# Optimization experiments

Hardware: AMD Instinct MI355X
Metric: run time of the kernel (lower is better)

Reference implementation:

```python
import jax, jax.numpy as jnp
import numpy as np

T, B, I, H = 512, 256, 256, 256


def setup_inputs() -> dict:
    key = jax.random.key(0)
    ks = jax.random.split(key, 4)
    s = 1.0 / np.sqrt(I + H)  # fan-in scaling like nn.Linear default
    return {
        "x": jax.random.normal(ks[0], (T, B, I), dtype=jnp.float32),
        "h": jnp.zeros((B, H), dtype=jnp.float32),
        "Wz_w": jax.random.normal(ks[1], (H, I + H), dtype=jnp.float32) * s,
        "Wz_b": jnp.zeros((H,), dtype=jnp.float32),
        "Wr_w": jax.random.normal(ks[2], (H, I + H), dtype=jnp.float32) * s,
        "Wr_b": jnp.zeros((H,), dtype=jnp.float32),
        "W_w": jax.random.normal(ks[3], (H, I + H), dtype=jnp.float32) * s,
        "W_b": jnp.zeros((H,), dtype=jnp.float32),
    }


def reference(x, h, Wz_w, Wz_b, Wr_w, Wr_b, W_w, W_b):
    # x: [T, B, I], h: [B, H]. Gate input order is cat(h, x) as in the torch code.
    def step(h, xt):
        gate = jnp.concatenate([h, xt], axis=1)              # [B, H+I]
        zt = jax.nn.sigmoid(gate @ Wz_w.T + Wz_b)            # [B, H]
        rt = jax.nn.sigmoid(gate @ Wr_w.T + Wr_b)            # [B, H]
        cand_in = jnp.concatenate([rt * h, xt], axis=1)      # [B, H+I]
        ht = (1.0 - zt) * h + zt * jnp.tanh(cand_in @ W_w.T + W_b)
        return ht, ht

    h_final, hAll = jax.lax.scan(step, h, x)                 # hAll: [T, B, H]
    return hAll, h_final
```

## Files before the change

### kernel.cpp

```cpp
#include <hip/hip_runtime.h>


typedef float f32x4 __attribute__((ext_vector_type(4)));
typedef short bf16x8 __attribute__((ext_vector_type(8)));

__device__ __forceinline__ unsigned short f2bf(float f) {
  union { float f; unsigned int u; } v; v.f = f;
  unsigned int u = v.u + 0x7fffu + ((v.u >> 16) & 1u);
  return (unsigned short)(u >> 16);
}
__device__ __forceinline__ float u2f(unsigned int u) {
  union { unsigned int u; float f; } v; v.u = u; return v.f;
}
__device__ __forceinline__ unsigned int cvt_pk_bf16(float lo, float hi) {
  unsigned int r;
  asm("v_cvt_pk_bf16_f32 %0, %1, %2" : "=v"(r) : "v"(lo), "v"(hi));
  return r;
}
__device__ __forceinline__ float sigmoid_f(float x) {
  return __builtin_amdgcn_rcpf(1.f + __expf(-x));
}
__device__ __forceinline__ float tanh_f(float x) {
  float e = __expf(2.f * x);
  return 1.f - 2.f * __builtin_amdgcn_rcpf(e + 1.f);
}
__device__ __forceinline__ f32x4 unpk(uint2 gv) {
  f32x4 a;
  a[0] = u2f(gv.x << 16); a[1] = u2f(gv.x & 0xffff0000u);
  a[2] = u2f(gv.y << 16); a[3] = u2f(gv.y & 0xffff0000u);
  return a;
}
__device__ __forceinline__ int frag_off(int j, int b) {
  return ((j >> 5) * 64 + ((j >> 3) & 3) * 16 + b) * 8 + (j & 7);
}

__global__ __launch_bounds__(256) void gru_gx_kernel(
    const float* __restrict__ x,
    const float* __restrict__ Wz, const float* __restrict__ Wr, const float* __restrict__ Wc,
    const float* __restrict__ bz, const float* __restrict__ br, const float* __restrict__ bc,
    unsigned short* __restrict__ gx)
{
  __shared__ __align__(16) unsigned short As[64][72];
  __shared__ __align__(16) unsigned short Bs[64][72];

  const int tid  = threadIdx.x;
  const int lane = tid & 63;
  const int wid  = tid >> 6;
  const int l15  = lane & 15;
  const int lg   = lane >> 4;
  const int m0   = blockIdx.x * 64;
  const int by   = blockIdx.y;
  const int gate = by >> 2;
  const int jb   = (by & 3) * 64;
  const float* W    = (gate == 0) ? Wz : ((gate == 1) ? Wr : Wc);
  const float* bias = (gate == 0) ? bz : ((gate == 1) ? br : bc);

  f32x4 acc[4];
  #pragma unroll
  for (int n = 0; n < 4; ++n) acc[n] = (f32x4){0.f, 0.f, 0.f, 0.f};

  for (int k0 = 0; k0 < 256; k0 += 64) {
    #pragma unroll
    for (int i = 0; i < 4; ++i) {
      int idx = tid + i * 256;
      int row = idx >> 4;
      int kq  = (idx & 15) << 2;
      float4 va = *(const float4*)(x + (size_t)(m0 + row) * 256 + k0 + kq);
      ushort4 ua; ua.x = f2bf(va.x); ua.y = f2bf(va.y); ua.z = f2bf(va.z); ua.w = f2bf(va.w);
      *(ushort4*)&As[row][kq] = ua;
      float4 vb = *(const float4*)(W + (size_t)(jb + row) * 512 + 256 + k0 + kq);
      ushort4 ub; ub.x = f2bf(vb.x); ub.y = f2bf(vb.y); ub.z = f2bf(vb.z); ub.w = f2bf(vb.w);
      *(ushort4*)&Bs[row][kq] = ub;
    }
    __syncthreads();
    #pragma unroll
    for (int ks = 0; ks < 64; ks += 32) {
      bf16x8 af = *(const bf16x8*)&As[wid * 16 + l15][ks + lg * 8];
      #pragma unroll
      for (int n = 0; n < 4; ++n) {
        bf16x8 bf = *(const bf16x8*)&Bs[n * 16 + l15][ks + lg * 8];
        acc[n] = __builtin_amdgcn_mfma_f32_16x16x32_bf16(af, bf, acc[n], 0, 0, 0);
      }
    }
    __syncthreads();
  }

  #pragma unroll
  for (int n = 0; n < 4; ++n) {
    float bv = bias[jb + n * 16 + l15];
    #pragma unroll
    for (int r = 0; r < 4; ++r) {
      As[wid * 16 + lg * 4 + r][n * 16 + l15] = f2bf(acc[n][r] + bv);
    }
  }
  __syncthreads();

  const int tt    = m0 >> 8;
  const int b0    = m0 & 255;
  const int jbase = by * 64;
  #pragma unroll
  for (int i = 0; i < 2; ++i) {
    int u    = tid + i * 256;
    int bg_l = u >> 7;
    int rem  = u & 127;
    int cb_l = rem >> 3;
    int bp   = rem & 7;
    int row0 = bg_l * 16 + bp * 2;
    uint2 lo = *(const uint2*)&As[row0][cb_l * 4];
    uint2 hi = *(const uint2*)&As[row0 + 1][cb_l * 4];
    uint4 val; val.x = lo.x; val.y = lo.y; val.z = hi.x; val.w = hi.y;
    size_t off = (((size_t)tt * 16 + (b0 >> 4) + bg_l) * 192 + (jbase >> 2) + cb_l) * 64
                 + (size_t)bp * 8;
    *(uint4*)(gx + off) = val;
  }
}

__global__ __launch_bounds__(512, 1) void gru_rec_kernel(
    const unsigned short* __restrict__ gx,
    const float* __restrict__ h0,
    const float* __restrict__ Wz, const float* __restrict__ Wr, const float* __restrict__ Wc,
    float* __restrict__ out)
{
  __shared__ __align__(16) float h_s[16][268];
  __shared__ __align__(16) float zt_s[16][268];
  __shared__ __align__(16) unsigned short hA[4096];
  __shared__ __align__(16) unsigned short rhA[4096];

  const int tid   = threadIdx.x;
  const int lane  = tid & 63;
  const int wid   = tid >> 6;
  const int l15   = lane & 15;
  const int lg    = lane >> 4;
  const int wg    = blockIdx.x;
  const int brow0 = wg * 16;

  bf16x8 w1[4][8];
  {
    const float* W  = (wid < 4) ? Wz : Wr;
    const int    cb = (wid & 3) * 64;
    #pragma unroll
    for (int n = 0; n < 4; ++n) {
      const int j = cb + n * 16 + l15;
      #pragma unroll
      for (int kk = 0; kk < 8; ++kk) {
        const int k = kk * 32 + lg * 8;
        const float* p = W + (size_t)j * 512 + k;
        float4 a = *(const float4*)p;
        float4 b = *(const float4*)(p + 4);
        bf16x8 f;
        f[0] = (short)f2bf(a.x); f[1] = (short)f2bf(a.y);
        f[2] = (short)f2bf(a.z); f[3] = (short)f2bf(a.w);
        f[4] = (short)f2bf(b.x); f[5] = (short)f2bf(b.y);
        f[6] = (short)f2bf(b.z); f[7] = (short)f2bf(b.w);
        w1[n][kk] = f;
      }
    }
  }
  bf16x8 w2[2][8];
  {
    const int cb = wid * 32;
    #pragma unroll
    for (int n = 0; n < 2; ++n) {
      const int j = cb + n * 16 + l15;
      #pragma unroll
      for (int kk = 0; kk < 8; ++kk) {
        const int k = kk * 32 + lg * 8;
        const float* p = Wc + (size_t)j * 512 + k;
        float4 a = *(const float4*)p;
        float4 b = *(const float4*)(p + 4);
        bf16x8 f;
        f[0] = (short)f2bf(a.x); f[1] = (short)f2bf(a.y);
        f[2] = (short)f2bf(a.z); f[3] = (short)f2bf(a.w);
        f[4] = (short)f2bf(b.x); f[5] = (short)f2bf(b.y);
        f[6] = (short)f2bf(b.z); f[7] = (short)f2bf(b.w);
        w2[n][kk] = f;
      }
    }
  }

  for (int idx = tid; idx < 16 * 256; idx += 512) {
    int r = idx >> 8, c = idx & 255;
    float v = h0[(size_t)(brow0 + r) * 256 + c];
    h_s[r][c] = v;
    hA[frag_off(c, r)] = f2bf(v);
  }

  uint2 g1[4], g2[2];
  {
    const size_t tb = (size_t)wg * 12288;
    #pragma unroll
    for (int n = 0; n < 4; ++n)
      g1[n] = *(const uint2*)(gx + tb + (size_t)(wid * 16 + n * 4 + lg) * 64 + l15 * 4);
    #pragma unroll
    for (int n = 0; n < 2; ++n)
      g2[n] = *(const uint2*)(gx + tb + (size_t)(128 + wid * 8 + n * 4 + lg) * 64 + l15 * 4);
  }
  __syncthreads();

  for (int t = 0; t < 512; ++t) {
    const int tn = (t < 511) ? (t + 1) : 511;
    const size_t tbn = ((size_t)tn * 16 + wg) * 12288;

    const int cb1 = wid * 64;
    f32x4 acc[4];
    #pragma unroll
    for (int n = 0; n < 4; ++n) acc[n] = unpk(g1[n]);
    #pragma unroll
    for (int n = 0; n < 4; ++n)
      g1[n] = *(const uint2*)(gx + tbn + (size_t)(wid * 16 + n * 4 + lg) * 64 + l15 * 4);

    #pragma unroll
    for (int kk = 0; kk < 8; ++kk) {
      bf16x8 hf = *(const bf16x8*)&hA[kk * 512 + lane * 8];
      #pragma unroll
      for (int n = 0; n < 4; ++n)
        acc[n] = __builtin_amdgcn_mfma_f32_16x16x32_bf16(w1[n][kk], hf, acc[n], 0, 0, 0);
    }
    if (wid < 4) {
      #pragma unroll
      for (int n = 0; n < 4; ++n) {
        const int c0 = cb1 + n * 16 + lg * 4;
        f32x4 zv;
        #pragma unroll
        for (int r = 0; r < 4; ++r) zv[r] = sigmoid_f(acc[n][r]);
        *(f32x4*)&zt_s[l15][c0] = zv;
      }
    } else {
      #pragma unroll
      for (int n = 0; n < 4; ++n) {
        const int c0h = (cb1 - 256) + n * 16 + lg * 4;
        f32x4 hv = *(const f32x4*)&h_s[l15][c0h];
        float rh0 = sigmoid_f(acc[n][0]) * hv[0];
        float rh1 = sigmoid_f(acc[n][1]) * hv[1];
        float rh2 = sigmoid_f(acc[n][2]) * hv[2];
        float rh3 = sigmoid_f(acc[n][3]) * hv[3];
        uint2 pk; pk.x = cvt_pk_bf16(rh0, rh1); pk.y = cvt_pk_bf16(rh2, rh3);
        *(uint2*)&rhA[frag_off(c0h, l15)] = pk;
      }
    }
    asm volatile("s_waitcnt lgkmcnt(0)" ::: "memory");
    __builtin_amdgcn_s_barrier();
    __builtin_amdgcn_sched_barrier(0);

    f32x4 acc2[2];
    #pragma unroll
    for (int n = 0; n < 2; ++n) acc2[n] = unpk(g2[n]);
    #pragma unroll
    for (int n = 0; n < 2; ++n)
      g2[n] = *(const uint2*)(gx + tbn + (size_t)(128 + wid * 8 + n * 4 + lg) * 64 + l15 * 4);

    #pragma unroll
    for (int kk = 0; kk < 8; ++kk) {
      bf16x8 rf = *(const bf16x8*)&rhA[kk * 512 + lane * 8];
      #pragma unroll
      for (int n = 0; n < 2; ++n)
        acc2[n] = __builtin_amdgcn_mfma_f32_16x16x32_bf16(w2[n][kk], rf, acc2[n], 0, 0, 0);
    }
    #pragma unroll
    for (int n = 0; n < 2; ++n) {
      const int j0 = wid * 32 + n * 16 + lg * 4;
      f32x4 zv = *(const f32x4*)&zt_s[l15][j0];
      f32x4 hp = *(const f32x4*)&h_s[l15][j0];
      f32x4 ht;
      #pragma unroll
      for (int r = 0; r < 4; ++r) {
        float th = tanh_f(acc2[n][r]);
        ht[r] = hp[r] + zv[r] * (th - hp[r]);
      }
      *(f32x4*)(out + (size_t)t * 65536 + (size_t)(brow0 + l15) * 256 + j0) = ht;
      if (t == 511)
        *(f32x4*)(out + (size_t)33554432 + (size_t)(brow0 + l15) * 256 + j0) = ht;
      *(f32x4*)&h_s[l15][j0] = ht;
      uint2 pk; pk.x = cvt_pk_bf16(ht[0], ht[1]); pk.y = cvt_pk_bf16(ht[2], ht[3]);
      *(uint2*)&hA[frag_off(j0, l15)] = pk;
    }
    asm volatile("s_waitcnt lgkmcnt(0)" ::: "memory");
    __builtin_amdgcn_s_barrier();
    __builtin_amdgcn_sched_barrier(0);
  }
}

extern "C" void kernel_launch(void* const* d_in, const int* in_sizes, int n_in,
                              void* d_out, int out_size, void* d_ws, size_t ws_size,
                              hipStream_t stream) {
  const float* x  = (const float*)d_in[0];
  const float* h0 = (const float*)d_in[1];
  const float* Wz = (const float*)d_in[2];
  const float* bz = (const float*)d_in[3];
  const float* Wr = (const float*)d_in[4];
  const float* br = (const float*)d_in[5];
  const float* Wc = (const float*)d_in[6];
  const float* bc = (const float*)d_in[7];
  float* out = (float*)d_out;
  unsigned short* gxbuf = (unsigned short*)d_ws;

  dim3 gridA(2048, 12);
  gru_gx_kernel<<<gridA, 256, 0, stream>>>(x, Wz, Wr, Wc, bz, br, bc, gxbuf);
  gru_rec_kernel<<<16, 512, 0, stream>>>(gxbuf, h0, Wz, Wr, Wc, out);
}
```

Baseline: 1.246 ms.

## Split recurrent GRU work across 16 waves per block instead of 8

Doubles the recurrent kernel's block size from 512 to 1024 threads. Each wave now handles half as many gate columns: two 16-column tiles for z/r and one for the candidate. This shortens the serial per-step MFMA chain and elementwise work per wave, aiming to cut latency on the 512-step critical path. In exchange, the two block-wide barriers per step cover twice as many waves, and only 16 blocks are launched, so most of the GPU stays idle.

```diff
diff --git a/kernel.cpp b/kernel.cpp
--- a/kernel.cpp
+++ b/kernel.cpp
@@ -115,7 +115,7 @@
   }
 }
 
-__global__ __launch_bounds__(512, 1) void gru_rec_kernel(
+__global__ __launch_bounds__(1024, 1) void gru_rec_kernel(
     const unsigned short* __restrict__ gx,
     const float* __restrict__ h0,
     const float* __restrict__ Wz, const float* __restrict__ Wr, const float* __restrict__ Wc,
@@ -129,17 +129,19 @@
   const int tid   = threadIdx.x;
   const int lane  = tid & 63;
   const int wid   = tid >> 6;
+  const int w7    = wid & 7;
+  const int zr    = wid >> 3;
   const int l15   = lane & 15;
   const int lg    = lane >> 4;
   const int wg    = blockIdx.x;
   const int brow0 = wg * 16;
 
-  bf16x8 w1[4][8];
+  bf16x8 w1[2][8];
   {
-    const float* W  = (wid < 4) ? Wz : Wr;
-    const int    cb = (wid & 3) * 64;
-    #pragma unroll
-    for (int n = 0; n < 4; ++n) {
+    const float* W  = zr ? Wr : Wz;
+    const int    cb = w7 * 32;
+    #pragma unroll
+    for (int n = 0; n < 2; ++n) {
       const int j = cb + n * 16 + l15;
       #pragma unroll
       for (int kk = 0; kk < 8; ++kk) {
@@ -156,44 +158,38 @@
       }
     }
   }
-  bf16x8 w2[2][8];
+  bf16x8 w2[8];
   {
-    const int cb = wid * 32;
-    #pragma unroll
-    for (int n = 0; n < 2; ++n) {
-      const int j = cb + n * 16 + l15;
-      #pragma unroll
-      for (int kk = 0; kk < 8; ++kk) {
-        const int k = kk * 32 + lg * 8;
-        const float* p = Wc + (size_t)j * 512 + k;
-        float4 a = *(const float4*)p;
-        float4 b = *(const float4*)(p + 4);
-        bf16x8 f;
-        f[0] = (short)f2bf(a.x); f[1] = (short)f2bf(a.y);
-        f[2] = (short)f2bf(a.z); f[3] = (short)f2bf(a.w);
-        f[4] = (short)f2bf(b.x); f[5] = (short)f2bf(b.y);
-        f[6] = (short)f2bf(b.z); f[7] = (short)f2bf(b.w);
-        w2[n][kk] = f;
-      }
-    }
-  }
-
-  for (int idx = tid; idx < 16 * 256; idx += 512) {
+    const int j = wid * 16 + l15;
+    #pragma unroll
+    for (int kk = 0; kk < 8; ++kk) {
+      const int k = kk * 32 + lg * 8;
+      const float* p = Wc + (size_t)j * 512 + k;
+      float4 a = *(const float4*)p;
+      float4 b = *(const float4*)(p + 4);
+      bf16x8 f;
+      f[0] = (short)f2bf(a.x); f[1] = (short)f2bf(a.y);
+      f[2] = (short)f2bf(a.z); f[3] = (short)f2bf(a.w);
+      f[4] = (short)f2bf(b.x); f[5] = (short)f2bf(b.y);
+      f[6] = (short)f2bf(b.z); f[7] = (short)f2bf(b.w);
+      w2[kk] = f;
+    }
+  }
+
+  for (int idx = tid; idx < 16 * 256; idx += 1024) {
     int r = idx >> 8, c = idx & 255;
     float v = h0[(size_t)(brow0 + r) * 256 + c];
     h_s[r][c] = v;
     hA[frag_off(c, r)] = f2bf(v);
   }
 
-  uint2 g1[4], g2[2];
+  uint2 g1[2], g2;
   {
     const size_t tb = (size_t)wg * 12288;
     #pragma unroll
-    for (int n = 0; n < 4; ++n)
-      g1[n] = *(const uint2*)(gx + tb + (size_t)(wid * 16 + n * 4 + lg) * 64 + l15 * 4);
-    #pragma unroll
     for (int n = 0; n < 2; ++n)
-      g2[n] = *(const uint2*)(gx + tb + (size_t)(128 + wid * 8 + n * 4 + lg) * 64 + l15 * 4);
+      g1[n] = *(const uint2*)(gx + tb + (size_t)(zr * 64 + w7 * 8 + n * 4 + lg) * 64 + l15 * 4);
+    g2 = *(const uint2*)(gx + tb + (size_t)(128 + wid * 4 + lg) * 64 + l15 * 4);
   }
   __syncthreads();
 
@@ -201,25 +197,24 @@
     const int tn = (t < 511) ? (t + 1) : 511;
     const size_t tbn = ((size_t)tn * 16 + wg) * 12288;
 
-    const int cb1 = wid * 64;
-    f32x4 acc[4];
-    #pragma unroll
-    for (int n = 0; n < 4; ++n) acc[n] = unpk(g1[n]);
-    #pragma unroll
-    for (int n = 0; n < 4; ++n)
-      g1[n] = *(const uint2*)(gx + tbn + (size_t)(wid * 16 + n * 4 + lg) * 64 + l15 * 4);
+    f32x4 acc[2];
+    #pragma unroll
+    for (int n = 0; n < 2; ++n) acc[n] = unpk(g1[n]);
+    #pragma unroll
+    for (int n = 0; n < 2; ++n)
+      g1[n] = *(const uint2*)(gx + tbn + (size_t)(zr * 64 + w7 * 8 + n * 4 + lg) * 64 + l15 * 4);
 
     #pragma unroll
     for (int kk = 0; kk < 8; ++kk) {
       bf16x8 hf = *(const bf16x8*)&hA[kk * 512 + lane * 8];
       #pragma unroll
-      for (int n = 0; n < 4; ++n)
+      for (int n = 0; n < 2; ++n)
         acc[n] = __builtin_amdgcn_mfma_f32_16x16x32_bf16(w1[n][kk], hf, acc[n], 0, 0, 0);
     }
-    if (wid < 4) {
-      #pragma unroll
-      for (int n = 0; n < 4; ++n) {
-        const int c0 = cb1 + n * 16 + lg * 4;
+    if (zr == 0) {
+      #pragma unroll
+      for (int n = 0; n < 2; ++n) {
+        const int c0 = w7 * 32 + n * 16 + lg * 4;
         f32x4 zv;
         #pragma unroll
         for (int r = 0; r < 4; ++r) zv[r] = sigmoid_f(acc[n][r]);
@@ -227,8 +222,8 @@
       }
     } else {
       #pragma unroll
-      for (int n = 0; n < 4; ++n) {
-        const int c0h = (cb1 - 256) + n * 16 + lg * 4;
+      for (int n = 0; n < 2; ++n) {
+        const int c0h = w7 * 32 + n * 16 + lg * 4;
         f32x4 hv = *(const f32x4*)&h_s[l15][c0h];
         float rh0 = sigmoid_f(acc[n][0]) * hv[0];
         float rh1 = sigmoid_f(acc[n][1]) * hv[1];
@@ -242,29 +237,22 @@
     __builtin_amdgcn_s_barrier();
     __builtin_amdgcn_sched_barrier(0);
 
-    f32x4 acc2[2];
-    #pragma unroll
-    for (int n = 0; n < 2; ++n) acc2[n] = unpk(g2[n]);
-    #pragma unroll
-    for (int n = 0; n < 2; ++n)
-      g2[n] = *(const uint2*)(gx + tbn + (size_t)(128 + wid * 8 + n * 4 + lg) * 64 + l15 * 4);
+    f32x4 acc2 = unpk(g2);
+    g2 = *(const uint2*)(gx + tbn + (size_t)(128 + wid * 4 + lg) * 64 + l15 * 4);
 
     #pragma unroll
     for (int kk = 0; kk < 8; ++kk) {
       bf16x8 rf = *(const bf16x8*)&rhA[kk * 512 + lane * 8];
-      #pragma unroll
-      for (int n = 0; n < 2; ++n)
-        acc2[n] = __builtin_amdgcn_mfma_f32_16x16x32_bf16(w2[n][kk], rf, acc2[n], 0, 0, 0);
-    }
-    #pragma unroll
-    for (int n = 0; n < 2; ++n) {
-      const int j0 = wid * 32 + n * 16 + lg * 4;
+      acc2 = __builtin_amdgcn_mfma_f32_16x16x32_bf16(w2[kk], rf, acc2, 0, 0, 0);
+    }
+    {
+      const int j0 = wid * 16 + lg * 4;
       f32x4 zv = *(const f32x4*)&zt_s[l15][j0];
       f32x4 hp = *(const f32x4*)&h_s[l15][j0];
       f32x4 ht;
       #pragma unroll
       for (int r = 0; r < 4; ++r) {
-        float th = tanh_f(acc2[n][r]);
+        float th = tanh_f(acc2[r]);
         ht[r] = hp[r] + zv[r] * (th - hp[r]);
       }
       *(f32x4*)(out + (size_t)t * 65536 + (size_t)(brow0 + l15) * 256 + j0) = ht;
@@ -296,5 +284,5 @@
 
   dim3 gridA(2048, 12);
   gru_gx_kernel<<<gridA, 256, 0, stream>>>(x, Wz, Wr, Wc, bz, br, bc, gxbuf);
-  gru_rec_kernel<<<16, 512, 0, stream>>>(gxbuf, h0, Wz, Wr, Wc, out);
-}
+  gru_rec_kernel<<<16, 1024, 0, stream>>>(gxbuf, h0, Wz, Wr, Wc, out);
+}
```

Result: slower. 1.448 ms (+16.2%).

## Repartition gate columns per wave so z, r and h stay in registers

Applied to the files above, without the earlier changes.

Each wave now owns the same 32 hidden columns for the z, r and candidate gates, instead of half the waves computing z and half computing r. Because of this, z and the fp32 hidden state stay in registers across the step, and the shared-memory h_s and zt_s arrays with their reads and writes are removed. The cost is more weight fragments held per wave and uniform sigmoid work in every wave, which raises register pressure.

```diff
diff --git a/kernel.cpp b/kernel.cpp
--- a/kernel.cpp
+++ b/kernel.cpp
@@ -121,8 +121,6 @@
     const float* __restrict__ Wz, const float* __restrict__ Wr, const float* __restrict__ Wc,
     float* __restrict__ out)
 {
-  __shared__ __align__(16) float h_s[16][268];
-  __shared__ __align__(16) float zt_s[16][268];
   __shared__ __align__(16) unsigned short hA[4096];
   __shared__ __align__(16) unsigned short rhA[4096];
 
@@ -133,17 +131,18 @@
   const int lg    = lane >> 4;
   const int wg    = blockIdx.x;
   const int brow0 = wg * 16;
-
-  bf16x8 w1[4][8];
-  {
-    const float* W  = (wid < 4) ? Wz : Wr;
-    const int    cb = (wid & 3) * 64;
-    #pragma unroll
-    for (int n = 0; n < 4; ++n) {
-      const int j = cb + n * 16 + l15;
-      #pragma unroll
-      for (int kk = 0; kk < 8; ++kk) {
-        const int k = kk * 32 + lg * 8;
+  const int cb    = wid * 32;
+
+  bf16x8 wz[2][8], wr[2][8], wc[2][8];
+  #pragma unroll
+  for (int n = 0; n < 2; ++n) {
+    const int j = cb + n * 16 + l15;
+    #pragma unroll
+    for (int kk = 0; kk < 8; ++kk) {
+      const int k = kk * 32 + lg * 8;
+      #pragma unroll
+      for (int g = 0; g < 3; ++g) {
+        const float* W = (g == 0) ? Wz : ((g == 1) ? Wr : Wc);
         const float* p = W + (size_t)j * 512 + k;
         float4 a = *(const float4*)p;
         float4 b = *(const float4*)(p + 4);
@@ -152,48 +151,29 @@
         f[2] = (short)f2bf(a.z); f[3] = (short)f2bf(a.w);
         f[4] = (short)f2bf(b.x); f[5] = (short)f2bf(b.y);
         f[6] = (short)f2bf(b.z); f[7] = (short)f2bf(b.w);
-        w1[n][kk] = f;
+        if (g == 0) wz[n][kk] = f; else if (g == 1) wr[n][kk] = f; else wc[n][kk] = f;
       }
     }
   }
-  bf16x8 w2[2][8];
-  {
-    const int cb = wid * 32;
-    #pragma unroll
-    for (int n = 0; n < 2; ++n) {
-      const int j = cb + n * 16 + l15;
-      #pragma unroll
-      for (int kk = 0; kk < 8; ++kk) {
-        const int k = kk * 32 + lg * 8;
-        const float* p = Wc + (size_t)j * 512 + k;
-        float4 a = *(const float4*)p;
-        float4 b = *(const float4*)(p + 4);
-        bf16x8 f;
-        f[0] = (short)f2bf(a.x); f[1] = (short)f2bf(a.y);
-        f[2] = (short)f2bf(a.z); f[3] = (short)f2bf(a.w);
-        f[4] = (short)f2bf(b.x); f[5] = (short)f2bf(b.y);
-        f[6] = (short)f2bf(b.z); f[7] = (short)f2bf(b.w);
-        w2[n][kk] = f;
-      }
-    }
-  }
-
+
+  f32x4 hreg[2];
+  #pragma unroll
+  for (int n = 0; n < 2; ++n)
+    hreg[n] = *(const f32x4*)(h0 + (size_t)(brow0 + l15) * 256 + cb + n * 16 + lg * 4);
   for (int idx = tid; idx < 16 * 256; idx += 512) {
     int r = idx >> 8, c = idx & 255;
-    float v = h0[(size_t)(brow0 + r) * 256 + c];
-    h_s[r][c] = v;
-    hA[frag_off(c, r)] = f2bf(v);
-  }
-
-  uint2 g1[4], g2[2];
+    hA[frag_off(c, r)] = f2bf(h0[(size_t)(brow0 + r) * 256 + c]);
+  }
+
+  uint2 g1z[2], g1r[2], g2[2];
   {
     const size_t tb = (size_t)wg * 12288;
     #pragma unroll
-    for (int n = 0; n < 4; ++n)
-      g1[n] = *(const uint2*)(gx + tb + (size_t)(wid * 16 + n * 4 + lg) * 64 + l15 * 4);
-    #pragma unroll
-    for (int n = 0; n < 2; ++n)
-      g2[n] = *(const uint2*)(gx + tb + (size_t)(128 + wid * 8 + n * 4 + lg) * 64 + l15 * 4);
+    for (int n = 0; n < 2; ++n) {
+      g1z[n] = *(const uint2*)(gx + tb + (size_t)(wid * 8 + n * 4 + lg) * 64 + l15 * 4);
+      g1r[n] = *(const uint2*)(gx + tb + (size_t)(64 + wid * 8 + n * 4 + lg) * 64 + l15 * 4);
+      g2[n]  = *(const uint2*)(gx + tb + (size_t)(128 + wid * 8 + n * 4 + lg) * 64 + l15 * 4);
+    }
   }
   __syncthreads();
 
@@ -201,42 +181,34 @@
     const int tn = (t < 511) ? (t + 1) : 511;
     const size_t tbn = ((size_t)tn * 16 + wg) * 12288;
 
-    const int cb1 = wid * 64;
-    f32x4 acc[4];
-    #pragma unroll
-    for (int n = 0; n < 4; ++n) acc[n] = unpk(g1[n]);
-    #pragma unroll
-    for (int n = 0; n < 4; ++n)
-      g1[n] = *(const uint2*)(gx + tbn + (size_t)(wid * 16 + n * 4 + lg) * 64 + l15 * 4);
+    f32x4 accZ[2], accR[2];
+    #pragma unroll
+    for (int n = 0; n < 2; ++n) { accZ[n] = unpk(g1z[n]); accR[n] = unpk(g1r[n]); }
+    #pragma unroll
+    for (int n = 0; n < 2; ++n) {
+      g1z[n] = *(const uint2*)(gx + tbn + (size_t)(wid * 8 + n * 4 + lg) * 64 + l15 * 4);
+      g1r[n] = *(const uint2*)(gx + tbn + (size_t)(64 + wid * 8 + n * 4 + lg) * 64 + l15 * 4);
+    }
 
     #pragma unroll
     for (int kk = 0; kk < 8; ++kk) {
       bf16x8 hf = *(const bf16x8*)&hA[kk * 512 + lane * 8];
-      #pragma unroll
-      for (int n = 0; n < 4; ++n)
-        acc[n] = __builtin_amdgcn_mfma_f32_16x16x32_bf16(w1[n][kk], hf, acc[n], 0, 0, 0);
-    }
-    if (wid < 4) {
-      #pragma unroll
-      for (int n = 0; n < 4; ++n) {
-        const int c0 = cb1 + n * 16 + lg * 4;
-        f32x4 zv;
-        #pragma unroll
-        for (int r = 0; r < 4; ++r) zv[r] = sigmoid_f(acc[n][r]);
-        *(f32x4*)&zt_s[l15][c0] = zv;
-      }
-    } else {
-      #pragma unroll
-      for (int n = 0; n < 4; ++n) {
-        const int c0h = (cb1 - 256) + n * 16 + lg * 4;
-        f32x4 hv = *(const f32x4*)&h_s[l15][c0h];
-        float rh0 = sigmoid_f(acc[n][0]) * hv[0];
-        float rh1 = sigmoid_f(acc[n][1]) * hv[1];
-        float rh2 = sigmoid_f(acc[n][2]) * hv[2];
-        float rh3 = sigmoid_f(acc[n][3]) * hv[3];
-        uint2 pk; pk.x = cvt_pk_bf16(rh0, rh1); pk.y = cvt_pk_bf16(rh2, rh3);
-        *(uint2*)&rhA[frag_off(c0h, l15)] = pk;
-      }
+      accZ[0] = __builtin_amdgcn_mfma_f32_16x16x32_bf16(wz[0][kk], hf, accZ[0], 0, 0, 0);
+      accZ[1] = __builtin_amdgcn_mfma_f32_16x16x32_bf16(wz[1][kk], hf, accZ[1], 0, 0, 0);
+      accR[0] = __builtin_amdgcn_mfma_f32_16x16x32_bf16(wr[0][kk], hf, accR[0], 0, 0, 0);
+      accR[1] = __builtin_amdgcn_mfma_f32_16x16x32_bf16(wr[1][kk], hf, accR[1], 0, 0, 0);
+    }
+    f32x4 zreg[2];
+    #pragma unroll
+    for (int n = 0; n < 2; ++n) {
+      #pragma unroll
+      for (int r = 0; r < 4; ++r) zreg[n][r] = sigmoid_f(accZ[n][r]);
+      float rh0 = sigmoid_f(accR[n][0]) * hreg[n][0];
+      float rh1 = sigmoid_f(accR[n][1]) * hreg[n][1];
+      float rh2 = sigmoid_f(accR[n][2]) * hreg[n][2];
+      float rh3 = sigmoid_f(accR[n][3]) * hreg[n][3];
+      uint2 pk; pk.x = cvt_pk_bf16(rh0, rh1); pk.y = cvt_pk_bf16(rh2, rh3);
+      *(uint2*)&rhA[frag_off(cb + n * 16 + lg * 4, l15)] = pk;
     }
     asm volatile("s_waitcnt lgkmcnt(0)" ::: "memory");
     __builtin_amdgcn_s_barrier();
@@ -252,27 +224,22 @@
     #pragma unroll
     for (int kk = 0; kk < 8; ++kk) {
       bf16x8 rf = *(const bf16x8*)&rhA[kk * 512 + lane * 8];
-      #pragma unroll
-      for (int n = 0; n < 2; ++n)
-        acc2[n] = __builtin_amdgcn_mfma_f32_16x16x32_bf16(w2[n][kk], rf, acc2[n], 0, 0, 0);
-    }
-    #pragma unroll
-    for (int n = 0; n < 2; ++n) {
-      const int j0 = wid * 32 + n * 16 + lg * 4;
-      f32x4 zv = *(const f32x4*)&zt_s[l15][j0];
-      f32x4 hp = *(const f32x4*)&h_s[l15][j0];
-      f32x4 ht;
+      acc2[0] = __builtin_amdgcn_mfma_f32_16x16x32_bf16(wc[0][kk], rf, acc2[0], 0, 0, 0);
+      acc2[1] = __builtin_amdgcn_mfma_f32_16x16x32_bf16(wc[1][kk], rf, acc2[1], 0, 0, 0);
+    }
+    #pragma unroll
+    for (int n = 0; n < 2; ++n) {
       #pragma unroll
       for (int r = 0; r < 4; ++r) {
         float th = tanh_f(acc2[n][r]);
-        ht[r] = hp[r] + zv[r] * (th - hp[r]);
+        hreg[n][r] = hreg[n][r] + zreg[n][r] * (th - hreg[n][r]);
       }
-      *(f32x4*)(out + (size_t)t * 65536 + (size_t)(brow0 + l15) * 256 + j0) = ht;
+      *(f32x4*)(out + (size_t)t * 65536 + (size_t)(brow0 + l15) * 256 + cb + n * 16 + lg * 4) = hreg[n];
       if (t == 511)
-        *(f32x4*)(out + (size_t)33554432 + (size_t)(brow0 + l15) * 256 + j0) = ht;
-      *(f32x4*)&h_s[l15][j0] = ht;
-      uint2 pk; pk.x = cvt_pk_bf16(ht[0], ht[1]); pk.y = cvt_pk_bf16(ht[2], ht[3]);
-      *(uint2*)&hA[frag_off(j0, l15)] = pk;
+        *(f32x4*)(out + (size_t)33554432 + (size_t)(brow0 + l15) * 256 + cb + n * 16 + lg * 4) = hreg[n];
+      uint2 pk; pk.x = cvt_pk_bf16(hreg[n][0], hreg[n][1]);
+      pk.y = cvt_pk_bf16(hreg[n][2], hreg[n][3]);
+      *(uint2*)&hA[frag_off(cb + n * 16 + lg * 4, l15)] = pk;
     }
     asm volatile("s_waitcnt lgkmcnt(0)" ::: "memory");
     __builtin_amdgcn_s_barrier();
```

Result: faster. 1.146 ms (-8.0%).
